# Kernel tuning notes

Hardware: AMD Instinct MI355X
Metric: run time of the kernel (lower is better)

## Reference

```python
import jax, jax.numpy as jnp
import numpy as np

X_LIST = [256, 256, 1024, 1024, 512]
LABEL_DIM = 8
MAX_SEQ_LEN = 64
B = 256
EMB = 128
ATTR = 64
HID = 512
LAYERS = 4


def setup_inputs() -> dict:
    key = jax.random.key(0)
    ki = iter(jax.random.split(key, 80))
    def nrm(shape):
        return jax.random.normal(next(ki), shape, jnp.float32) * 0.02
    inp = {}
    inp['label'] = jax.random.normal(next(ki), (B, LABEL_DIM), jnp.float32)
    inp['length'] = jax.random.randint(next(ki), (B,), 1, MAX_SEQ_LEN + 1)
    inp['x'] = jnp.stack([jax.random.randint(next(ki), (B, MAX_SEQ_LEN), 0, v) for v in X_LIST], axis=-1)
    inp['x_now'] = jnp.stack([jax.random.randint(next(ki), (B, MAX_SEQ_LEN), 0, v) for v in X_LIST], axis=-1)
    for i, v in enumerate(X_LIST):
        inp[f'emb{i}'] = nrm((v, EMB))
    inp['pad_emb'] = jnp.zeros((1, ATTR), jnp.float32)
    for i in range(len(X_LIST) - 1):
        inp[f'cond_W{i}'] = nrm((ATTR, (i + 1) * EMB))
        inp[f'cond_b{i}'] = jnp.zeros((ATTR,), jnp.float32)
    inp['len_W'] = nrm((64, MAX_SEQ_LEN))
    inp['len_b'] = jnp.zeros((64,), jnp.float32)
    comb_in = EMB * len(X_LIST) + 64  # 704
    inp['comb_W'] = nrm((LABEL_DIM, HID, comb_in))
    inp['comb_b'] = jnp.zeros((LABEL_DIM, HID), jnp.float32)
    inp['lstm_Wih'] = nrm((LAYERS, 4 * HID, HID))
    inp['lstm_Whh'] = nrm((LAYERS, 4 * HID, HID))
    inp['lstm_bih'] = jnp.zeros((LAYERS, 4 * HID), jnp.float32)
    inp['lstm_bhh'] = jnp.zeros((LAYERS, 4 * HID), jnp.float32)
    for i, v in enumerate(X_LIST):
        inp[f'out_W{i}'] = nrm((v, HID + ATTR))
        inp[f'out_b{i}'] = jnp.zeros((v,), jnp.float32)
    return inp


def _forward(label, emb0, emb1, emb2, emb3, emb4, pad_emb,
             cond_W0, cond_W1, cond_W2, cond_W3, cond_b0, cond_b1, cond_b2, cond_b3,
             len_W, len_b, comb_W, comb_b,
             lstm_Wih, lstm_Whh, lstm_bih, lstm_bhh,
             out_W0, out_W1, out_W2, out_W3, out_W4,
             out_b0, out_b1, out_b2, out_b3, out_b4,
             length, x, x_now):
    embs = [emb0, emb1, emb2, emb3, emb4]
    cond_W = [cond_W0, cond_W1, cond_W2, cond_W3]
    cond_b = [cond_b0, cond_b1, cond_b2, cond_b3]
    out_W = [out_W0, out_W1, out_W2, out_W3, out_W4]
    out_b = [out_b0, out_b1, out_b2, out_b3, out_b4]
    Bn, T, _ = x.shape
    # length branch: one_hot(length-1) -> Linear -> ReLU -> [B, 64]
    length_oh = jax.nn.one_hot(length - 1, MAX_SEQ_LEN, dtype=jnp.float32)
    length_out = jax.nn.relu(length_oh @ len_W.T + len_b)
    # per-attribute embedding lookups, concat -> [B, T, 5*128]
    emb_list = jnp.concatenate([embs[i][x[:, :, i]] for i in range(len(X_LIST))], axis=2)
    now_emb = jnp.concatenate([embs[i][x_now[:, :, i]] for i in range(len(X_LIST) - 1)], axis=2)
    # condition features: pad for head 0, small MLPs on prefixes of now_emb
    attr = [jnp.broadcast_to(pad_emb, (Bn, T, ATTR))]
    for i in range(len(X_LIST) - 1):
        attr.append(jax.nn.relu(now_emb[:, :, :(i + 1) * EMB] @ cond_W[i].T + cond_b[i]))
    combined = jnp.concatenate(
        [emb_list, jnp.broadcast_to(length_out[:, None, :], (Bn, T, 64))], axis=2)  # [B,T,704]
    # label-routed combine_fc: compute all LABEL_DIM branches, gather matching branch
    fc = jax.nn.relu(jnp.einsum('btd,lhd->blth', combined, comb_W) + comb_b[None, :, None, :])
    label_int = jnp.argmax(label, axis=1)
    combined_out = jnp.take_along_axis(fc, label_int[:, None, None, None], axis=1)[:, 0]  # [B,T,H]
    # 4-layer LSTM, torch gate order (i,f,g,o), zero initial state
    xs = combined_out.transpose(1, 0, 2)  # [T,B,H]
    for l in range(LAYERS):
        Wih_T = lstm_Wih[l].T
        Whh_T = lstm_Whh[l].T
        bias = lstm_bih[l] + lstm_bhh[l]
        def step(carry, xt, Wih_T=Wih_T, Whh_T=Whh_T, bias=bias):
            h, c = carry
            g = xt @ Wih_T + h @ Whh_T + bias
            gi, gf, gg, go = jnp.split(g, 4, axis=-1)
            c = jax.nn.sigmoid(gf) * c + jax.nn.sigmoid(gi) * jnp.tanh(gg)
            h = jax.nn.sigmoid(go) * jnp.tanh(c)
            return (h, c), h
        z = jnp.zeros((Bn, HID), xs.dtype)
        _, xs = jax.lax.scan(step, (z, z), xs)
    hidden = xs.transpose(1, 0, 2)  # [B,T,H]
    # per-attribute log-softmax heads over [hidden ; attr_i]
    preds = [jax.nn.log_softmax(
        jnp.concatenate([hidden, attr[i]], axis=-1) @ out_W[i].T + out_b[i], axis=-1)
        for i in range(len(X_LIST))]
    return jnp.concatenate(preds, axis=-1)  # [B, T, sum(X_LIST)]


def reference(label, emb0, emb1, emb2, emb3, emb4, pad_emb,
              cond_W0, cond_W1, cond_W2, cond_W3, cond_b0, cond_b1, cond_b2, cond_b3,
              len_W, len_b, comb_W, comb_b,
              lstm_Wih, lstm_Whh, lstm_bih, lstm_bhh,
              out_W0, out_W1, out_W2, out_W3, out_W4,
              out_b0, out_b1, out_b2, out_b3, out_b4,
              length, x, x_now):
    return _forward(label, emb0, emb1, emb2, emb3, emb4, pad_emb,
                    cond_W0, cond_W1, cond_W2, cond_W3, cond_b0, cond_b1, cond_b2, cond_b3,
                    len_W, len_b, comb_W, comb_b,
                    lstm_Wih, lstm_Whh, lstm_bih, lstm_bhh,
                    out_W0, out_W1, out_W2, out_W3, out_W4,
                    out_b0, out_b1, out_b2, out_b3, out_b4,
                    length, x, x_now)
```

## Files before the change

kernel.cpp:

```cpp
#include <hip/hip_runtime.h>
#include <math.h>


#define B_    256
#define T_    64
#define EMB_  128
#define HID_  512
#define G4_   2048
#define CIN_  704
#define HA_   576
#define ROW_  3072
#define OFF_HA 2048
#define OFF_HB 2560

#define WKB_   516
#define WKC_   4128
#define HB0_   33024
#define SMEM_F 37120

#define BAR_T(tau) (64 + (tau) * 32)

struct Params {
  const float* label; const int* length; const int* x; const int* xnow;
  const float* emb[5]; const float* pad;
  const float* condW[4]; const float* condB[4];
  const float* lenW; const float* lenB;
  const float* combW; const float* combB;
  const float* Wih; const float* Whh; const float* bih; const float* bhh;
  const float* outW[5]; const float* outB[5];
  unsigned int* bar;
  float* out;
};

__device__ __forceinline__ void multi_barrier(unsigned int* cnt, unsigned int* gen,
                                              unsigned int n) {
  __syncthreads();
  if (threadIdx.x == 0) {
    unsigned int g = __hip_atomic_load(gen, __ATOMIC_RELAXED, __HIP_MEMORY_SCOPE_AGENT);
    unsigned int a = __hip_atomic_fetch_add(cnt, 1u, __ATOMIC_ACQ_REL, __HIP_MEMORY_SCOPE_AGENT);
    if (a == n - 1u) {
      __hip_atomic_store(cnt, 0u, __ATOMIC_RELAXED, __HIP_MEMORY_SCOPE_AGENT);
      __hip_atomic_store(gen, g + 1u, __ATOMIC_RELEASE, __HIP_MEMORY_SCOPE_AGENT);
    } else {
      while (__hip_atomic_load(gen, __ATOMIC_RELAXED, __HIP_MEMORY_SCOPE_AGENT) == g) {
        __builtin_amdgcn_s_sleep(2);
      }
      (void)__hip_atomic_load(gen, __ATOMIC_ACQUIRE, __HIP_MEMORY_SCOPE_AGENT);
    }
  }
  __syncthreads();
}

#define WRSLAB(SL) do { \
  _Pragma("unroll") \
  for (int qq = 0; qq < 16; ++qq) { \
    int cc = ((qq + lo) & 15) * 4; \
    *(float4*)&(SL)[lo * 64 + cc] = \
      make_float4(acc[qq >> 1][(qq & 1) * 4 + 0], acc[qq >> 1][(qq & 1) * 4 + 1], \
                  acc[qq >> 1][(qq & 1) * 4 + 2], acc[qq >> 1][(qq & 1) * 4 + 3]); \
  } } while (0)

#define RDSLAB(SL) do { \
  _Pragma("unroll") \
  for (int qq = 0; qq < 16; ++qq) { \
    int cc = ((qq + lo) & 15) * 4; \
    float4 vv = *(const float4*)&(SL)[lo * 64 + cc]; \
    acc[qq >> 1][(qq & 1) * 4 + 0] += vv.x; acc[qq >> 1][(qq & 1) * 4 + 1] += vv.y; \
    acc[qq >> 1][(qq & 1) * 4 + 2] += vv.z; acc[qq >> 1][(qq & 1) * 4 + 3] += vv.w; \
  } } while (0)

__global__ __launch_bounds__(256) void k_t1(Params P, int l) {
  __shared__ float sm[4608];
  const int out_off = (l & 1) ? OFF_HA : OFF_HB;
  const float* Wih = P.Wih + (size_t)l * G4_ * HID_;
  const int tid = threadIdx.x, blk = blockIdx.x;
  const int rt = blk >> 4, kt = blk & 15;
  const int r0 = rt * 128, k0 = kt * 32;
  const int ul = tid >> 3, kl = (tid & 7) * 4;
  #pragma unroll
  for (int p = 0; p < 4; ++p) {
    float4 v = *(const float4*)(Wih + (size_t)(r0 + p * 32 + ul) * HID_ + k0 + kl);
    *(float4*)&sm[(p * 32 + ul) * 36 + kl] = v;
  }
  __syncthreads();
  const int kk = tid >> 3, qb = (tid & 7) * 4;
  #pragma unroll
  for (int p = 0; p < 4; ++p) {
    int rl = qb + p * 32;
    float4 v = make_float4(sm[(rl + 0) * 36 + kk], sm[(rl + 1) * 36 + kk],
                           sm[(rl + 2) * 36 + kk], sm[(rl + 3) * 36 + kk]);
    int kabs = k0 + kk;
    int row = (r0 >> 8) * 256 + (kabs >> 1);
    int col = out_off + (kabs & 1) * 256 + (r0 & 255) + rl;
    *(float4*)&P.out[(size_t)row * ROW_ + col] = v;
  }
}

__global__ __launch_bounds__(256, 3) void k_gih(Params P, int l) {
  const int in_off  = (l & 1) ? OFF_HB : OFF_HA;
  const int out_off = (l & 1) ? OFF_HA : OFF_HB;
  const int tid = threadIdx.x;
  const int rg = tid & 63, mh = tid >> 6;
  const int rb = blockIdx.x >> 1, ch = blockIdx.x & 1;
  const int m_base = rb * 32;
  const float* arow[8];
  #pragma unroll
  for (int mm = 0; mm < 8; ++mm)
    arow[mm] = P.out + (size_t)(m_base + mh * 8 + mm) * ROW_ + in_off;
  for (int p0 = 0; p0 < 4; ++p0) {
    const int p = ch * 4 + p0;
    float acc[4][8];
    #pragma unroll
    for (int c = 0; c < 4; ++c)
      #pragma unroll
      for (int m = 0; m < 8; ++m) acc[c][m] = 0.f;
    const float* wp = P.out + (size_t)(p * 256) * ROW_ + out_off + rg * 4;
    for (int kq = 0; kq < 64; ++kq) {
      float4 w0 = *(const float4*)(wp);
      float4 w1 = *(const float4*)(wp + 256);
      float4 w2 = *(const float4*)(wp + ROW_);
      float4 w3 = *(const float4*)(wp + ROW_ + 256);
      #pragma unroll
      for (int mm = 0; mm < 8; ++mm) {
        float4 a = *(const float4*)(arow[mm] + kq * 4);
        acc[0][mm] += w0.x * a.x + w1.x * a.y + w2.x * a.z + w3.x * a.w;
        acc[1][mm] += w0.y * a.x + w1.y * a.y + w2.y * a.z + w3.y * a.w;
        acc[2][mm] += w0.z * a.x + w1.z * a.y + w2.z * a.z + w3.z * a.w;
        acc[3][mm] += w0.w * a.x + w1.w * a.y + w2.w * a.z + w3.w * a.w;
      }
      wp += 2 * ROW_;
    }
    int r4 = p * 256 + rg * 4;
    float4 bi = *(const float4*)(P.bih + l * G4_ + r4);
    float4 bh = *(const float4*)(P.bhh + l * G4_ + r4);
    float bx = bi.x + bh.x, by = bi.y + bh.y, bz = bi.z + bh.z, bw = bi.w + bh.w;
    #pragma unroll
    for (int mm = 0; mm < 8; ++mm) {
      int m = m_base + mh * 8 + mm;
      *(float4*)&P.out[(size_t)m * ROW_ + r4] =
        make_float4(acc[0][mm] + bx, acc[1][mm] + by,
                    acc[2][mm] + bz, acc[3][mm] + bw);
    }
  }
}

__global__ __launch_bounds__(256, 1) void k_lstmB(Params P, int l) {
  __shared__ float smem[SMEM_F];
  unsigned int* bar = P.bar;
  const int tid = threadIdx.x;
  const int blk = blockIdx.x;
  const int team = blk & 7, member = blk >> 3;
  const int out_off = (l & 1) ? OFF_HA : OFF_HB;

  const int kb  = tid >> 5;
  const int sgq = (tid >> 3) & 3;
  const int rg  = tid & 7;
  const bool owner = (tid < 32);
  const int s_base = team * 32 + sgq * 8;
  const int ucol0  = member * 16 + rg * 2;

  {
    const float* Wl = P.Whh + (size_t)l * G4_ * HID_;
    const int r = tid >> 2, q = tid & 3;
    const float* src = Wl + (size_t)((r & 3) * 512 + member * 16 + (r >> 2)) * HID_
                       + q * 128;
    for (int j = 0; j < 32; ++j) {
      float4 v = *(const float4*)(src + j * 4);
      int k0 = q * 128 + j * 4;
      #pragma unroll
      for (int e = 0; e < 4; ++e) {
        int k = k0 + e;
        smem[(k >> 6) * WKC_ + ((k >> 3) & 7) * WKB_ + (k & 7) * 64 + r] = (&v.x)[e];
      }
    }
  }
  __syncthreads();

  float cst[8][2];

  if (owner) {
    #pragma unroll
    for (int sj = 0; sj < 8; ++sj) {
      const size_t grow = (size_t)((s_base + sj) * 64 + 0) * ROW_;
      float2 zi2 = *(const float2*)&P.out[grow + 0 * 512 + ucol0];
      float2 zg2 = *(const float2*)&P.out[grow + 2 * 512 + ucol0];
      float2 zo2 = *(const float2*)&P.out[grow + 3 * 512 + ucol0];
      #pragma unroll
      for (int uj = 0; uj < 2; ++uj) {
        float zi = (&zi2.x)[uj], zg = (&zg2.x)[uj], zo = (&zo2.x)[uj];
        float si = 1.f / (1.f + expf(-zi));
        float so = 1.f / (1.f + expf(-zo));
        float cn = si * tanhf(zg);
        cst[sj][uj] = cn;
        P.out[grow + out_off + ucol0 + uj] = so * tanhf(cn);
      }
    }
  }

  for (int t = 1; t < T_; ++t) {
    multi_barrier(&bar[BAR_T(team)], &bar[BAR_T(team) + 16], 32);

    float Gp[8][4][2];
    if (owner) {
      #pragma unroll
      for (int sj = 0; sj < 8; ++sj) {
        const size_t grow = (size_t)((s_base + sj) * 64 + t) * ROW_;
        #pragma unroll
        for (int g = 0; g < 4; ++g) {
          float2 v = *(const float2*)&P.out[grow + g * 512 + ucol0];
          Gp[sj][g][0] = v.x; Gp[sj][g][1] = v.y;
        }
      }
    }

    float acc[8][8];
    #pragma unroll
    for (int a = 0; a < 8; ++a)
      #pragma unroll
      for (int b = 0; b < 8; ++b) acc[a][b] = 0.f;

    const int idx0 = tid * 2, idx1 = idx0 + 1;
    const int s0 = idx0 >> 4, kq0 = idx0 & 15;
    const int s1 = idx1 >> 4, kq1 = idx1 & 15;
    const size_t hrow0 = (size_t)((team * 32 + s0) * 64 + (t - 1)) * ROW_ + out_off;
    const size_t hrow1 = (size_t)((team * 32 + s1) * 64 + (t - 1)) * ROW_ + out_off;
    const int c0 = s0 * 64 + ((kq0 * 4 + 8 * (s0 >> 3)) & 63);
    const int c1 = s1 * 64 + ((kq1 * 4 + 8 * (s1 >> 3)) & 63);
    {
      float4 v0 = *(const float4*)&P.out[hrow0 + kq0 * 4];
      float4 v1 = *(const float4*)&P.out[hrow1 + kq1 * 4];
      *(float4*)&smem[HB0_ + c0] = v0;
      *(float4*)&smem[HB0_ + c1] = v1;
    }
    __syncthreads();

    for (int kc = 0; kc < 8; ++kc) {
      float4 nv0 = make_float4(0.f, 0.f, 0.f, 0.f), nv1 = nv0;
      if (kc < 7) {
        nv0 = *(const float4*)&P.out[hrow0 + (kc + 1) * 64 + kq0 * 4];
        nv1 = *(const float4*)&P.out[hrow1 + (kc + 1) * 64 + kq1 * 4];
      }
      const float* wp  = &smem[kc * WKC_ + kb * WKB_ + rg * 8];
      const float* hbv = &smem[HB0_ + (kc & 1) * 2048];
      #pragma unroll
      for (int kq2 = 0; kq2 < 2; ++kq2) {
        float4 h4[8];
        const int colr = kb * 8 + kq2 * 4;
        #pragma unroll
        for (int sj = 0; sj < 8; ++sj)
          h4[sj] = *(const float4*)&hbv[(sgq * 8 + sj) * 64 + ((colr + 8 * sgq) & 63)];
        #pragma unroll
        for (int e = 0; e < 4; ++e) {
          const float4 wA = *(const float4*)&wp[(kq2 * 4 + e) * 64];
          const float4 wB = *(const float4*)&wp[(kq2 * 4 + e) * 64 + 4];
          #pragma unroll
          for (int sj = 0; sj < 8; ++sj) {
            const float hv = (&h4[sj].x)[e];
            acc[sj][0] += hv * wA.x; acc[sj][1] += hv * wA.y;
            acc[sj][2] += hv * wA.z; acc[sj][3] += hv * wA.w;
            acc[sj][4] += hv * wB.x; acc[sj][5] += hv * wB.y;
            acc[sj][6] += hv * wB.z; acc[sj][7] += hv * wB.w;
          }
        }
      }
      if (kc < 7) {
        *(float4*)&smem[HB0_ + ((kc + 1) & 1) * 2048 + c0] = nv0;
        *(float4*)&smem[HB0_ + ((kc + 1) & 1) * 2048 + c1] = nv1;
      }
      __syncthreads();
    }

    #pragma unroll
    for (int a = 0; a < 8; ++a)
      #pragma unroll
      for (int b = 0; b < 8; ++b)
        acc[a][b] += __shfl_xor(acc[a][b], 32, 64);
    const int wv = tid >> 6;
    const bool halfLo = ((tid >> 5) & 1) == 0;
    const int lo = tid & 31;
    float* slab0 = &smem[HB0_];
    float* slab1 = &smem[HB0_ + 2048];
    if (halfLo && wv == 1) WRSLAB(slab0);
    if (halfLo && wv == 3) WRSLAB(slab1);
    __syncthreads();
    if (halfLo && wv == 0) RDSLAB(slab0);
    if (halfLo && wv == 2) RDSLAB(slab1);
    __syncthreads();
    if (halfLo && wv == 2) WRSLAB(slab0);
    __syncthreads();
    if (owner) {
      RDSLAB(slab0);
      #pragma unroll
      for (int sj = 0; sj < 8; ++sj) {
        const size_t orow = (size_t)((s_base + sj) * 64 + t) * ROW_;
        #pragma unroll
        for (int uj = 0; uj < 2; ++uj) {
          float zi = Gp[sj][0][uj] + acc[sj][uj * 4 + 0];
          float zf = Gp[sj][1][uj] + acc[sj][uj * 4 + 1];
          float zg = Gp[sj][2][uj] + acc[sj][uj * 4 + 2];
          float zo = Gp[sj][3][uj] + acc[sj][uj * 4 + 3];
          float si = 1.f / (1.f + expf(-zi));
          float sf = 1.f / (1.f + expf(-zf));
          float so = 1.f / (1.f + expf(-zo));
          float cn = sf * cst[sj][uj] + si * tanhf(zg);
          cst[sj][uj] = cn;
          P.out[orow + out_off + ucol0 + uj] = so * tanhf(cn);
        }
      }
    }
  }
}

__global__ __launch_bounds__(256) void k_combine(Params P) {
  __shared__ float sA[16][CIN_];
  __shared__ float sLen[64];
  int b = blockIdx.x >> 2, t0 = (blockIdx.x & 3) * 16;
  int tid = threadIdx.x;
  int li = P.length[b] - 1;
  if (tid < 64) {
    float v = P.lenW[tid * 64 + li] + P.lenB[tid];
    sLen[tid] = v > 0.f ? v : 0.f;
  }
  float best = P.label[b * 8]; int l = 0;
  #pragma unroll
  for (int k = 1; k < 8; ++k) {
    float lv = P.label[b * 8 + k];
    if (lv > best) { best = lv; l = k; }
  }
  __syncthreads();
  for (int tt = 0; tt < 16; ++tt) {
    int t = t0 + tt;
    for (int k = tid; k < CIN_; k += 256) {
      float v;
      if (k < 640) {
        int a = k >> 7, e = k & 127;
        int xi = P.x[((b * T_ + t) * 5) + a];
        v = P.emb[a][xi * EMB_ + e];
      } else {
        v = sLen[k - 640];
      }
      sA[tt][k] = v;
    }
  }
  __syncthreads();
  int hg = tid & 127, mh = tid >> 7;
  int h = hg * 4, tb = mh * 8;
  const float* W0 = P.combW + ((size_t)(l * HID_ + h)) * CIN_;
  float acc[4][8];
  #pragma unroll
  for (int c = 0; c < 4; ++c)
    #pragma unroll
    for (int m = 0; m < 8; ++m) acc[c][m] = 0.f;
  for (int k = 0; k < CIN_; k += 4) {
    float4 w0 = *(const float4*)(const void*)(W0 + k);
    float4 w1 = *(const float4*)(const void*)(W0 + CIN_ + k);
    float4 w2 = *(const float4*)(const void*)(W0 + 2 * CIN_ + k);
    float4 w3 = *(const float4*)(const void*)(W0 + 3 * CIN_ + k);
    #pragma unroll
    for (int m = 0; m < 8; ++m) {
      float4 av = *(const float4*)&sA[tb + m][k];
      acc[0][m] += w0.x*av.x + w0.y*av.y + w0.z*av.z + w0.w*av.w;
      acc[1][m] += w1.x*av.x + w1.y*av.y + w1.z*av.z + w1.w*av.w;
      acc[2][m] += w2.x*av.x + w2.y*av.y + w2.z*av.z + w2.w*av.w;
      acc[3][m] += w3.x*av.x + w3.y*av.y + w3.z*av.z + w3.w*av.w;
    }
  }
  #pragma unroll
  for (int c = 0; c < 4; ++c) {
    float bias = P.combB[l * HID_ + h + c];
    #pragma unroll
    for (int m = 0; m < 8; ++m) {
      float v = acc[c][m] + bias;
      P.out[((size_t)(b * T_ + t0 + tb + m)) * ROW_ + OFF_HA + h + c] = v > 0.f ? v : 0.f;
    }
  }
}

template<int HEAD, int VH, int OFF>
__global__ __launch_bounds__(256, 2) void k_head(Params P) {
  __shared__ float sB[32][512];
  __shared__ float sAt[32][64];
  const int tid = threadIdx.x;
  const int m0 = blockIdx.x * 32;
  if (HEAD == 0) {
    for (int i = tid; i < 32 * 64; i += 256) sAt[i >> 6][i & 63] = P.pad[i & 63];
  } else {
    const int KA = HEAD * EMB_;
    for (int i = tid; i < 32 * KA; i += 256) {
      int tt = i / KA, k = i - tt * KA;
      int a = k >> 7, e = k & 127;
      int xi = P.xnow[((m0 + tt) * 5) + a];
      sB[tt][k] = P.emb[a][xi * EMB_ + e];
    }
    __syncthreads();
    int rg = tid >> 6, j = tid & 63;
    const float* Wr = P.condW[HEAD - 1] + (size_t)j * KA;
    float acc[8] = {0.f,0.f,0.f,0.f,0.f,0.f,0.f,0.f};
    for (int k = 0; k < KA; k += 4) {
      float4 w = *(const float4*)(const void*)(Wr + k);
      #pragma unroll
      for (int m = 0; m < 8; ++m) {
        float4 av = *(const float4*)&sB[rg * 8 + m][k];
        acc[m] += w.x*av.x + w.y*av.y + w.z*av.z + w.w*av.w;
      }
    }
    float bias = P.condB[HEAD - 1][j];
    #pragma unroll
    for (int m = 0; m < 8; ++m) {
      float v = acc[m] + bias;
      sAt[rg * 8 + m][j] = v > 0.f ? v : 0.f;
    }
    __syncthreads();
  }
  for (int i = tid; i < 32 * 512; i += 256) {
    int tt = i >> 9, k = i & 511;
    sB[tt][k] = P.out[((size_t)(m0 + tt)) * ROW_ + OFF_HA + k];
  }
  __syncthreads();
  constexpr int CG  = (VH >= 512) ? 128 : 64;
  constexpr int RPG = (VH >= 512) ? 16 : 8;
  const int cg = tid & (CG - 1), mh = tid / CG;
  const int tb = mh * RPG;
  const float* Wb = P.outW[HEAD];
  const float* bs = P.outB[HEAD];
  for (int c0 = cg * 4; c0 < VH; c0 += CG * 4) {
    const float* Wr = Wb + (size_t)c0 * HA_;
    float acc2[4][RPG];
    #pragma unroll
    for (int c = 0; c < 4; ++c)
      #pragma unroll
      for (int m = 0; m < RPG; ++m) acc2[c][m] = 0.f;
    for (int k = 0; k < 512; k += 4) {
      float4 w0 = *(const float4*)(const void*)(Wr + k);
      float4 w1 = *(const float4*)(const void*)(Wr + HA_ + k);
      float4 w2 = *(const float4*)(const void*)(Wr + 2 * HA_ + k);
      float4 w3 = *(const float4*)(const void*)(Wr + 3 * HA_ + k);
      #pragma unroll
      for (int m = 0; m < RPG; ++m) {
        float4 av = *(const float4*)&sB[tb + m][k];
        acc2[0][m] += w0.x*av.x + w0.y*av.y + w0.z*av.z + w0.w*av.w;
        acc2[1][m] += w1.x*av.x + w1.y*av.y + w1.z*av.z + w1.w*av.w;
        acc2[2][m] += w2.x*av.x + w2.y*av.y + w2.z*av.z + w2.w*av.w;
        acc2[3][m] += w3.x*av.x + w3.y*av.y + w3.z*av.z + w3.w*av.w;
      }
    }
    for (int k = 0; k < 64; k += 4) {
      float4 w0 = *(const float4*)(const void*)(Wr + 512 + k);
      float4 w1 = *(const float4*)(const void*)(Wr + HA_ + 512 + k);
      float4 w2 = *(const float4*)(const void*)(Wr + 2 * HA_ + 512 + k);
      float4 w3 = *(const float4*)(const void*)(Wr + 3 * HA_ + 512 + k);
      #pragma unroll
      for (int m = 0; m < RPG; ++m) {
        float4 av = *(const float4*)&sAt[tb + m][k];
        acc2[0][m] += w0.x*av.x + w0.y*av.y + w0.z*av.z + w0.w*av.w;
        acc2[1][m] += w1.x*av.x + w1.y*av.y + w1.z*av.z + w1.w*av.w;
        acc2[2][m] += w2.x*av.x + w2.y*av.y + w2.z*av.z + w2.w*av.w;
        acc2[3][m] += w3.x*av.x + w3.y*av.y + w3.z*av.z + w3.w*av.w;
      }
    }
    #pragma unroll
    for (int c = 0; c < 4; ++c) {
      float bi = bs[c0 + c];
      #pragma unroll
      for (int m = 0; m < RPG; ++m)
        P.out[((size_t)(m0 + tb + m)) * ROW_ + OFF + c0 + c] = acc2[c][m] + bi;
    }
  }
}

__global__ __launch_bounds__(256) void k_lsm(Params P) {
  __shared__ float sred[4];
  int m = blockIdx.x;
  float* row0 = P.out + (size_t)m * ROW_;
  int tid = threadIdx.x, lane = tid & 63, wid = tid >> 6;
  const int V[5] = {256, 256, 1024, 1024, 512};
  int off = 0;
  for (int head = 0; head < 5; ++head) {
    float* row = row0 + off; int Vh = V[head];
    float mx = -1e30f;
    for (int c = tid; c < Vh; c += 256) mx = fmaxf(mx, row[c]);
    for (int o = 32; o > 0; o >>= 1) mx = fmaxf(mx, __shfl_down(mx, o, 64));
    if (lane == 0) sred[wid] = mx;
    __syncthreads();
    mx = fmaxf(fmaxf(sred[0], sred[1]), fmaxf(sred[2], sred[3]));
    __syncthreads();
    float s = 0.f;
    for (int c = tid; c < Vh; c += 256) s += expf(row[c] - mx);
    for (int o = 32; o > 0; o >>= 1) s += __shfl_down(s, o, 64);
    if (lane == 0) sred[wid] = s;
    __syncthreads();
    float lse = mx + logf(sred[0] + sred[1] + sred[2] + sred[3]);
    __syncthreads();
    for (int c = tid; c < Vh; c += 256) row[c] = row[c] - lse;
    off += Vh;
  }
}

extern "C" void kernel_launch(void* const* d_in, const int* in_sizes, int n_in,
                              void* d_out, int out_size, void* d_ws, size_t ws_size,
                              hipStream_t stream) {
  (void)in_sizes; (void)n_in; (void)out_size; (void)ws_size;
  Params P;
  P.label  = (const float*)d_in[0];
  P.length = (const int*)  d_in[1];
  P.x      = (const int*)  d_in[2];
  P.xnow   = (const int*)  d_in[3];
  for (int i = 0; i < 5; ++i) P.emb[i] = (const float*)d_in[4 + i];
  P.pad = (const float*)d_in[9];
  for (int i = 0; i < 4; ++i) {
    P.condW[i] = (const float*)d_in[10 + 2 * i];
    P.condB[i] = (const float*)d_in[11 + 2 * i];
  }
  P.lenW  = (const float*)d_in[18]; P.lenB  = (const float*)d_in[19];
  P.combW = (const float*)d_in[20]; P.combB = (const float*)d_in[21];
  P.Wih   = (const float*)d_in[22]; P.Whh   = (const float*)d_in[23];
  P.bih   = (const float*)d_in[24]; P.bhh   = (const float*)d_in[25];
  for (int i = 0; i < 5; ++i) {
    P.outW[i] = (const float*)d_in[26 + 2 * i];
    P.outB[i] = (const float*)d_in[27 + 2 * i];
  }
  P.bar = (unsigned int*)d_ws;
  P.out = (float*)d_out;

  hipMemsetAsync(d_ws, 0, 1536, stream);
  k_combine<<<1024, 256, 0, stream>>>(P);
  for (int l = 0; l < 4; ++l) {
    k_t1 <<<256,  256, 0, stream>>>(P, l);
    k_gih<<<1024, 256, 0, stream>>>(P, l);
    void* args[] = { &P, &l };
    hipLaunchCooperativeKernel((void*)k_lstmB, dim3(256), dim3(256), args, 0, stream);
  }
  k_head<0,  256,    0><<<512, 256, 0, stream>>>(P);
  k_head<1,  256,  256><<<512, 256, 0, stream>>>(P);
  k_head<2, 1024,  512><<<512, 256, 0, stream>>>(P);
  k_head<4,  512, 2560><<<512, 256, 0, stream>>>(P);
  k_head<3, 1024, 1536><<<512, 256, 0, stream>>>(P);
  k_lsm<<<16384, 256, 0, stream>>>(P);
}
```

Baseline: 11.85 ms.

## Split recurrent LSTM kernel across 512 blocks with 8 hidden units each

The cooperative recurrent kernel now launches 512 blocks instead of 256. Each block owns 8 hidden units instead of 16, so its Whh slice in shared memory and its per-step accumulator set are halved, and two blocks can reside per CU. The aim is to cut the per-step matvec latency on the serial time loop. In exchange each team barrier now synchronises 64 blocks instead of 32, and every block still reloads the full previous hidden state for its 32 sequences, so redundant global traffic doubles.

Measured after the change: 12.69 ms. 7.1% more time.

```diff
diff --git a/kernel.cpp b/kernel.cpp
--- a/kernel.cpp
+++ b/kernel.cpp
@@ -13,10 +13,10 @@
 #define OFF_HA 2048
 #define OFF_HB 2560
 
-#define WKB_   516
-#define WKC_   4128
-#define HB0_   33024
-#define SMEM_F 37120
+#define WSUB_  256
+#define WKC_   2048
+#define HB0_   16384
+#define SMEM_F 20480
 
 #define BAR_T(tau) (64 + (tau) * 32)
 
@@ -53,20 +53,19 @@
 
 #define WRSLAB(SL) do { \
   _Pragma("unroll") \
-  for (int qq = 0; qq < 16; ++qq) { \
-    int cc = ((qq + lo) & 15) * 4; \
-    *(float4*)&(SL)[lo * 64 + cc] = \
-      make_float4(acc[qq >> 1][(qq & 1) * 4 + 0], acc[qq >> 1][(qq & 1) * 4 + 1], \
-                  acc[qq >> 1][(qq & 1) * 4 + 2], acc[qq >> 1][(qq & 1) * 4 + 3]); \
+  for (int qq = 0; qq < 8; ++qq) { \
+    int cc = ((qq + lo) & 7) * 4; \
+    *(float4*)&(SL)[lo * 32 + cc] = \
+      make_float4(acc[qq][0], acc[qq][1], acc[qq][2], acc[qq][3]); \
   } } while (0)
 
 #define RDSLAB(SL) do { \
   _Pragma("unroll") \
-  for (int qq = 0; qq < 16; ++qq) { \
-    int cc = ((qq + lo) & 15) * 4; \
-    float4 vv = *(const float4*)&(SL)[lo * 64 + cc]; \
-    acc[qq >> 1][(qq & 1) * 4 + 0] += vv.x; acc[qq >> 1][(qq & 1) * 4 + 1] += vv.y; \
-    acc[qq >> 1][(qq & 1) * 4 + 2] += vv.z; acc[qq >> 1][(qq & 1) * 4 + 3] += vv.w; \
+  for (int qq = 0; qq < 8; ++qq) { \
+    int cc = ((qq + lo) & 7) * 4; \
+    float4 vv = *(const float4*)&(SL)[lo * 32 + cc]; \
+    acc[qq][0] += vv.x; acc[qq][1] += vv.y; \
+    acc[qq][2] += vv.z; acc[qq][3] += vv.w; \
   } } while (0)
 
 __global__ __launch_bounds__(256) void k_t1(Params P, int l) {
@@ -144,7 +143,7 @@
   }
 }
 
-__global__ __launch_bounds__(256, 1) void k_lstmB(Params P, int l) {
+__global__ __launch_bounds__(256, 2) void k_lstmB(Params P, int l) {
   __shared__ float smem[SMEM_F];
   unsigned int* bar = P.bar;
   const int tid = threadIdx.x;
@@ -157,67 +156,61 @@
   const int rg  = tid & 7;
   const bool owner = (tid < 32);
   const int s_base = team * 32 + sgq * 8;
-  const int ucol0  = member * 16 + rg * 2;
+  const int ucol0  = member * 8 + rg;
 
   {
     const float* Wl = P.Whh + (size_t)l * G4_ * HID_;
-    const int r = tid >> 2, q = tid & 3;
-    const float* src = Wl + (size_t)((r & 3) * 512 + member * 16 + (r >> 2)) * HID_
-                       + q * 128;
-    for (int j = 0; j < 32; ++j) {
+    const int r = tid >> 3, q = tid & 7;
+    const float* src = Wl + (size_t)((r & 3) * 512 + member * 8 + (r >> 2)) * HID_
+                       + q * 64;
+    for (int j = 0; j < 16; ++j) {
       float4 v = *(const float4*)(src + j * 4);
-      int k0 = q * 128 + j * 4;
+      int k0 = q * 64 + j * 4;
       #pragma unroll
       for (int e = 0; e < 4; ++e) {
         int k = k0 + e;
-        smem[(k >> 6) * WKC_ + ((k >> 3) & 7) * WKB_ + (k & 7) * 64 + r] = (&v.x)[e];
-      }
-    }
-  }
-  __syncthreads();
-
-  float cst[8][2];
+        smem[(k >> 6) * WKC_ + ((k >> 3) & 7) * WSUB_ + (k & 7) * 32 + r] = (&v.x)[e];
+      }
+    }
+  }
+  __syncthreads();
+
+  float cst[8];
 
   if (owner) {
     #pragma unroll
     for (int sj = 0; sj < 8; ++sj) {
       const size_t grow = (size_t)((s_base + sj) * 64 + 0) * ROW_;
-      float2 zi2 = *(const float2*)&P.out[grow + 0 * 512 + ucol0];
-      float2 zg2 = *(const float2*)&P.out[grow + 2 * 512 + ucol0];
-      float2 zo2 = *(const float2*)&P.out[grow + 3 * 512 + ucol0];
-      #pragma unroll
-      for (int uj = 0; uj < 2; ++uj) {
-        float zi = (&zi2.x)[uj], zg = (&zg2.x)[uj], zo = (&zo2.x)[uj];
-        float si = 1.f / (1.f + expf(-zi));
-        float so = 1.f / (1.f + expf(-zo));
-        float cn = si * tanhf(zg);
-        cst[sj][uj] = cn;
-        P.out[grow + out_off + ucol0 + uj] = so * tanhf(cn);
-      }
+      float zi = P.out[grow + 0 * 512 + ucol0];
+      float zg = P.out[grow + 2 * 512 + ucol0];
+      float zo = P.out[grow + 3 * 512 + ucol0];
+      float si = 1.f / (1.f + expf(-zi));
+      float so = 1.f / (1.f + expf(-zo));
+      float cn = si * tanhf(zg);
+      cst[sj] = cn;
+      P.out[grow + out_off + ucol0] = so * tanhf(cn);
     }
   }
 
   for (int t = 1; t < T_; ++t) {
-    multi_barrier(&bar[BAR_T(team)], &bar[BAR_T(team) + 16], 32);
-
-    float Gp[8][4][2];
+    multi_barrier(&bar[BAR_T(team)], &bar[BAR_T(team) + 16], 64);
+
+    float Gp[8][4];
     if (owner) {
       #pragma unroll
       for (int sj = 0; sj < 8; ++sj) {
         const size_t grow = (size_t)((s_base + sj) * 64 + t) * ROW_;
         #pragma unroll
-        for (int g = 0; g < 4; ++g) {
-          float2 v = *(const float2*)&P.out[grow + g * 512 + ucol0];
-          Gp[sj][g][0] = v.x; Gp[sj][g][1] = v.y;
-        }
-      }
-    }
-
-    float acc[8][8];
+        for (int g = 0; g < 4; ++g)
+          Gp[sj][g] = P.out[grow + g * 512 + ucol0];
+      }
+    }
+
+    float acc[8][4];
     #pragma unroll
     for (int a = 0; a < 8; ++a)
       #pragma unroll
-      for (int b = 0; b < 8; ++b) acc[a][b] = 0.f;
+      for (int b = 0; b < 4; ++b) acc[a][b] = 0.f;
 
     const int idx0 = tid * 2, idx1 = idx0 + 1;
     const int s0 = idx0 >> 4, kq0 = idx0 & 15;
@@ -240,7 +233,7 @@
         nv0 = *(const float4*)&P.out[hrow0 + (kc + 1) * 64 + kq0 * 4];
         nv1 = *(const float4*)&P.out[hrow1 + (kc + 1) * 64 + kq1 * 4];
       }
-      const float* wp  = &smem[kc * WKC_ + kb * WKB_ + rg * 8];
+      const float* wp  = &smem[kc * WKC_ + kb * WSUB_ + rg * 4];
       const float* hbv = &smem[HB0_ + (kc & 1) * 2048];
       #pragma unroll
       for (int kq2 = 0; kq2 < 2; ++kq2) {
@@ -251,15 +244,12 @@
           h4[sj] = *(const float4*)&hbv[(sgq * 8 + sj) * 64 + ((colr + 8 * sgq) & 63)];
         #pragma unroll
         for (int e = 0; e < 4; ++e) {
-          const float4 wA = *(const float4*)&wp[(kq2 * 4 + e) * 64];
-          const float4 wB = *(const float4*)&wp[(kq2 * 4 + e) * 64 + 4];
+          const float4 wv = *(const float4*)&wp[(kq2 * 4 + e) * 32];
           #pragma unroll
           for (int sj = 0; sj < 8; ++sj) {
             const float hv = (&h4[sj].x)[e];
-            acc[sj][0] += hv * wA.x; acc[sj][1] += hv * wA.y;
-            acc[sj][2] += hv * wA.z; acc[sj][3] += hv * wA.w;
-            acc[sj][4] += hv * wB.x; acc[sj][5] += hv * wB.y;
-            acc[sj][6] += hv * wB.z; acc[sj][7] += hv * wB.w;
+            acc[sj][0] += hv * wv.x; acc[sj][1] += hv * wv.y;
+            acc[sj][2] += hv * wv.z; acc[sj][3] += hv * wv.w;
           }
         }
       }
@@ -273,13 +263,13 @@
     #pragma unroll
     for (int a = 0; a < 8; ++a)
       #pragma unroll
-      for (int b = 0; b < 8; ++b)
+      for (int b = 0; b < 4; ++b)
         acc[a][b] += __shfl_xor(acc[a][b], 32, 64);
     const int wv = tid >> 6;
     const bool halfLo = ((tid >> 5) & 1) == 0;
     const int lo = tid & 31;
     float* slab0 = &smem[HB0_];
-    float* slab1 = &smem[HB0_ + 2048];
+    float* slab1 = &smem[HB0_ + 1024];
     if (halfLo && wv == 1) WRSLAB(slab0);
     if (halfLo && wv == 3) WRSLAB(slab1);
     __syncthreads();
@@ -293,19 +283,16 @@
       #pragma unroll
       for (int sj = 0; sj < 8; ++sj) {
         const size_t orow = (size_t)((s_base + sj) * 64 + t) * ROW_;
-        #pragma unroll
-        for (int uj = 0; uj < 2; ++uj) {
-          float zi = Gp[sj][0][uj] + acc[sj][uj * 4 + 0];
-          float zf = Gp[sj][1][uj] + acc[sj][uj * 4 + 1];
-          float zg = Gp[sj][2][uj] + acc[sj][uj * 4 + 2];
-          float zo = Gp[sj][3][uj] + acc[sj][uj * 4 + 3];
-          float si = 1.f / (1.f + expf(-zi));
-          float sf = 1.f / (1.f + expf(-zf));
-          float so = 1.f / (1.f + expf(-zo));
-          float cn = sf * cst[sj][uj] + si * tanhf(zg);
-          cst[sj][uj] = cn;
-          P.out[orow + out_off + ucol0 + uj] = so * tanhf(cn);
-        }
+        float zi = Gp[sj][0] + acc[sj][0];
+        float zf = Gp[sj][1] + acc[sj][1];
+        float zg = Gp[sj][2] + acc[sj][2];
+        float zo = Gp[sj][3] + acc[sj][3];
+        float si = 1.f / (1.f + expf(-zi));
+        float sf = 1.f / (1.f + expf(-zf));
+        float so = 1.f / (1.f + expf(-zo));
+        float cn = sf * cst[sj] + si * tanhf(zg);
+        cst[sj] = cn;
+        P.out[orow + out_off + ucol0] = so * tanhf(cn);
       }
     }
   }
@@ -528,7 +515,7 @@
     k_t1 <<<256,  256, 0, stream>>>(P, l);
     k_gih<<<1024, 256, 0, stream>>>(P, l);
     void* args[] = { &P, &l };
-    hipLaunchCooperativeKernel((void*)k_lstmB, dim3(256), dim3(256), args, 0, stream);
+    hipLaunchCooperativeKernel((void*)k_lstmB, dim3(512), dim3(256), args, 0, stream);
   }
   k_head<0,  256,    0><<<512, 256, 0, stream>>>(P);
   k_head<1,  256,  256><<<512, 256, 0, stream>>>(P);
```
